# Optimization experiments

Hardware: AMD Instinct MI355X
Metric: run time of the kernel (lower is better)

The kernel has to match this reference:

```python
import jax, jax.numpy as jnp
import numpy as np
import math

DIM, SCALES, ORIENTS, K = 32, 3, 8, 15
SIGMA, GAMMA = 5.0, 0.5
B, H, W = 4, 128, 128

def _make_gabor_filters():
    # matches EnhancedBlockGabor._create_complex_filters
    coords = np.arange(-(K // 2), K // 2 + 1, dtype=np.float32)
    y, x = np.meshgrid(coords, coords, indexing='ij')  # torch.meshgrid default 'ij'
    filts = []
    for s in range(SCALES):
        fu = 1.0 / 2 ** s
        for o in range(ORIENTS):
            theta = o * math.pi / ORIENTS
            xt = x * math.cos(theta) + y * math.sin(theta)
            yt = -x * math.sin(theta) + y * math.cos(theta)
            env = np.exp(-(xt ** 2 + GAMMA ** 2 * yt ** 2) / (2 * SIGMA ** 2))
            amp = fu ** 2 / (math.pi * GAMMA ** 2)
            real = amp * env * np.cos(2 * math.pi * fu * xt)
            imag = amp * env * np.sin(2 * math.pi * fu * xt)
            filts.append(np.stack([real, imag]))
    return jnp.asarray(np.stack(filts), dtype=jnp.float32)  # (S*O, 2, K, K)

def setup_inputs() -> dict:
    key = jax.random.key(0)
    k1, k2, k3 = jax.random.split(key, 3)
    x = jax.random.normal(k1, (B, DIM, H, W), dtype=jnp.float32)
    filters = _make_gabor_filters()
    cin = DIM * SCALES * ORIENTS
    w1 = jax.random.normal(k2, (DIM, cin), dtype=jnp.float32) / np.sqrt(cin)
    b1 = jax.random.normal(k3, (DIM,), dtype=jnp.float32) * 0.01
    return {"x": x, "filters": filters, "w1": w1, "b1": b1}

def reference(x, filters, w1, b1):
    Bb, C, Hh, Ww = x.shape
    SO = filters.shape[0]
    pad = K // 2
    # depthwise multi-scale Gabor conv: every channel vs every (scale,orient,re/im) filter
    xr = x.reshape(Bb * C, 1, Hh, Ww)
    kern = filters.reshape(SO * 2, 1, K, K)
    feat = jax.lax.conv_general_dilated(
        xr, kern, window_strides=(1, 1), padding=[(pad, pad), (pad, pad)],
        dimension_numbers=('NCHW', 'OIHW', 'NCHW'))  # (B*C, SO*2, H, W)
    feat = feat.reshape(Bb, C, SO, 2, Hh, Ww)
    mag = jnp.sqrt(feat[:, :, :, 0] ** 2 + feat[:, :, :, 1] ** 2)  # (B,C,SO,H,W)
    mag = jnp.swapaxes(mag, -1, -2)  # original permutes H<->W before reshape
    mag = mag.reshape(Bb, C * SO, Hh, Ww)
    y = jnp.einsum('oc,bchw->bohw', w1, mag) + b1[None, :, None, None]
    mean = y.mean(axis=(2, 3), keepdims=True)
    var = y.var(axis=(2, 3), keepdims=True)
    return (y - mean) / jnp.sqrt(var + 1e-5)  # InstanceNorm2d (affine=False)
```

## Files before the change

kernel.cpp:

```cpp
#include <hip/hip_runtime.h>


typedef __attribute__((ext_vector_type(8))) short bfx8;
typedef __attribute__((ext_vector_type(4))) float fx4;
typedef __attribute__((ext_vector_type(4))) unsigned ux4;

#define NREP   2
#define RPITCH 144
#define RROWS  144
#define IMG_SH (RROWS * RPITCH)
#define REP_SH (128 * IMG_SH)
#define XREP_SH (NREP * REP_SH)

#define A_OFF    ((size_t)XREP_SH * 2)
#define W1B_OFF  (A_OFF + (size_t)48 * 256 * 2)
#define YP_OFF   (W1B_OFF + (size_t)32 * 32 * 32 * 2)
#define ST_OFF   (YP_OFF + (size_t)128 * 16384 * 4)

#define STG_REP_DW 1296
#define STG_BUF_DW (2 * STG_REP_DW)

__device__ __forceinline__ unsigned short f2bf(float f) {
    unsigned u = __float_as_uint(f);
    u = (u + 0x7FFFu + ((u >> 16) & 1u)) >> 16;
    return (unsigned short)u;
}

__global__ void prep(const float* __restrict__ x, const float* __restrict__ filt,
                     const float* __restrict__ w1, unsigned* __restrict__ xrep,
                     unsigned short* __restrict__ A, unsigned short* __restrict__ w1b,
                     float* __restrict__ stats)
{
    const int bid = blockIdx.x;
    if (bid < 2048) {
        const int DW_PER_ROW = RPITCH / 2;
        const int DW_PER_IMG = IMG_SH / 2;
        const int DW_PER_REP = REP_SH / 2;
        const int total = NREP * DW_PER_REP;
        for (int i = bid * 256 + threadIdx.x; i < total; i += 2048 * 256) {
            int phi  = i / DW_PER_REP;
            int rem  = i - phi * DW_PER_REP;
            int img  = rem / DW_PER_IMG;
            int rem2 = rem - img * DW_PER_IMG;
            int r    = rem2 / DW_PER_ROW;
            int pd   = rem2 - r * DW_PER_ROW;
            int c0   = 2 * pd + phi;
            float v0 = 0.f, v1 = 0.f;
            int rr = r - 7;
            if (rr >= 0 && rr < 128) {
                const float* row = x + ((size_t)img * 128 + rr) * 128;
                int cc0 = c0 - 7;
                if (cc0 >= 0 && cc0 < 128) v0 = row[cc0];
                int cc1 = c0 - 6;
                if (cc1 >= 0 && cc1 < 128) v1 = row[cc1];
            }
            xrep[i] = (unsigned)f2bf(v0) | ((unsigned)f2bf(v1) << 16);
        }
    } else {
        int t = (bid - 2048) * 256 + threadIdx.x;
        if (t < 48 * 256) {
            int f = t >> 8, k = t & 255;
            int ky = k >> 4, kx = k & 15;
            float v = 0.f;
            if (ky < 15 && kx < 15) v = filt[(f * 15 + ky) * 15 + kx];
            A[t] = f2bf(v);
        } else if (t < 48 * 256 + 32 * 32 * 32) {
            int j = t - 48 * 256;
            int c = j >> 10, o = (j >> 5) & 31, so = j & 31;
            float v = (so < 24) ? w1[o * 768 + c * 24 + so] : 0.f;
            w1b[j] = f2bf(v);
        } else if (t < 48 * 256 + 32 * 32 * 32 + 256) {
            stats[t - (48 * 256 + 32 * 32 * 32)] = 0.f;
        }
    }
}

__global__ void __attribute__((amdgpu_waves_per_eu(2, 2)))
__launch_bounds__(256)
conv_mix(const unsigned short* __restrict__ xrep,
         const unsigned short* __restrict__ Aw,
         const unsigned short* __restrict__ w1b,
         float* __restrict__ ypart, float* __restrict__ stats)
{
    __shared__ unsigned stagew[2 * STG_BUF_DW];
    __shared__ unsigned mag_lds[4][32][20];
    __shared__ float stat_lds[4][4][16];

    const int tid  = threadIdx.x;
    const int lane = tid & 63;
    const int wave = tid >> 6;
    const int n    = lane & 15;
    const int q    = lane >> 4;

    const int bid = blockIdx.x;
    const int b   = (bid >> 1) & 3;
    const int h   = (bid & 1) * 64 + (bid >> 3);

    if (lane < 32) {
        ux4 z4 = {0u, 0u, 0u, 0u};
        *(ux4*)&mag_lds[wave][lane][12] = z4;
    }

    ux4 afr[3][8];
#pragma unroll
    for (int mt = 0; mt < 3; ++mt)
#pragma unroll
        for (int s = 0; s < 8; ++s)
            afr[mt][s] = *(const ux4*)(Aw + ((mt * 16 + n) * 256 + s * 32 + q * 8));
#pragma unroll
    for (int mt = 0; mt < 3; ++mt)
#pragma unroll
        for (int s = 0; s < 8; ++s)
            asm volatile("" : "+v"(afr[mt][s]));

    const int px0 = wave * 32;
    const int p   = n & 1;
    const int fbase = p * STG_REP_DW + (q >> 1) * 72 +
                      ((px0 + (n - p) + 8 * (q & 1)) >> 1);

    const int s1p  = (tid + 256) >= 288;
    const int off1 = tid + 256 - (s1p ? 288 : 0);
    const size_t ib0 = ((size_t)(b * 32) * RROWS + h) * RPITCH;

    const fx4 zero4 = {0.f, 0.f, 0.f, 0.f};
    fx4 yacc[2][2];
#pragma unroll
    for (int mt = 0; mt < 2; ++mt)
#pragma unroll
        for (int t = 0; t < 2; ++t) yacc[mt][t] = zero4;

    {
        const unsigned short* g = xrep + ib0;
        ux4 v0 = *(const ux4*)(g + tid * 8);
        ux4 v1 = *(const ux4*)(g + (size_t)s1p * REP_SH + off1 * 8);
        ux4 v2 = {0u, 0u, 0u, 0u};
        if (tid < 64) v2 = *(const ux4*)(g + REP_SH + (tid + 224) * 8);
        *(ux4*)&stagew[tid * 4] = v0;
        *(ux4*)&stagew[s1p * STG_REP_DW + off1 * 4] = v1;
        if (tid < 64) *(ux4*)&stagew[STG_REP_DW + (tid + 224) * 4] = v2;
    }
    __syncthreads();

    for (int c = 0; c < 32; ++c) {
        ux4 nv0, nv1, nv2;
        if (c < 31) {
            const unsigned short* g = xrep + ib0 + (size_t)(c + 1) * IMG_SH;
            nv0 = *(const ux4*)(g + tid * 8);
            nv1 = *(const ux4*)(g + (size_t)s1p * REP_SH + off1 * 8);
            if (tid < 64) nv2 = *(const ux4*)(g + REP_SH + (tid + 224) * 8);
        }

        bfx8 wf[2];
#pragma unroll
        for (int mt = 0; mt < 2; ++mt)
            wf[mt] = *(const bfx8*)(w1b + ((c * 32 + mt * 16 + n) * 32 + q * 8));

        const int fb = (c & 1) * STG_BUF_DW + fbase;
        ux4 braw[2][8];
#pragma unroll
        for (int s = 0; s < 8; ++s)
#pragma unroll
            for (int t = 0; t < 2; ++t) {
                const int ix = fb + s * 144 + t * 8;
                ux4 v = {stagew[ix], stagew[ix + 1], stagew[ix + 2], stagew[ix + 3]};
                braw[t][s] = v;
            }
#pragma unroll
        for (int s = 0; s < 8; ++s)
#pragma unroll
            for (int t = 0; t < 2; ++t)
                asm volatile("" : "+v"(braw[t][s]));

        fx4 cacc[3][2];
#pragma unroll
        for (int mt = 0; mt < 3; ++mt)
#pragma unroll
            for (int t = 0; t < 2; ++t) cacc[mt][t] = zero4;

#pragma unroll
        for (int s = 0; s < 8; ++s)
#pragma unroll
            for (int t = 0; t < 2; ++t) {
                bfx8 bf = __builtin_bit_cast(bfx8, braw[t][s]);
#pragma unroll
                for (int mt = 0; mt < 3; ++mt)
                    cacc[mt][t] = __builtin_amdgcn_mfma_f32_16x16x32_bf16(
                        __builtin_bit_cast(bfx8, afr[mt][s]), bf, cacc[mt][t], 0, 0, 0);
            }

#pragma unroll
        for (int t = 0; t < 2; ++t)
#pragma unroll
            for (int mt = 0; mt < 3; ++mt) {
                float m0 = sqrtf(cacc[mt][t][0] * cacc[mt][t][0] +
                                 cacc[mt][t][1] * cacc[mt][t][1]);
                float m1 = sqrtf(cacc[mt][t][2] * cacc[mt][t][2] +
                                 cacc[mt][t][3] * cacc[mt][t][3]);
                unsigned u0 = __float_as_uint(m0), u1 = __float_as_uint(m1);
                unsigned pk = ((u0 + 0x8000u) >> 16) | ((u1 + 0x8000u) & 0xFFFF0000u);
                mag_lds[wave][t * 16 + n][4 * mt + q] = pk;
            }

#pragma unroll
        for (int t = 0; t < 2; ++t) {
            ux4 raw = *(const ux4*)&mag_lds[wave][t * 16 + n][q * 4];
            bfx8 mb = __builtin_bit_cast(bfx8, raw);
#pragma unroll
            for (int mt = 0; mt < 2; ++mt)
                yacc[mt][t] = __builtin_amdgcn_mfma_f32_16x16x32_bf16(
                    wf[mt], mb, yacc[mt][t], 0, 0, 0);
        }

        if (c < 31) {
            const int wb = ((c + 1) & 1) * STG_BUF_DW;
            *(ux4*)&stagew[wb + tid * 4] = nv0;
            *(ux4*)&stagew[wb + s1p * STG_REP_DW + off1 * 4] = nv1;
            if (tid < 64) *(ux4*)&stagew[wb + STG_REP_DW + (tid + 224) * 4] = nv2;
        }
        __syncthreads();
    }

    float* yp = ypart + (size_t)(b * 32) * 16384 + h * 128;
#pragma unroll
    for (int mt = 0; mt < 2; ++mt)
#pragma unroll
        for (int t = 0; t < 2; ++t) {
            const int w0 = px0 + t * 16 + n;
#pragma unroll
            for (int r = 0; r < 4; ++r)
                yp[(size_t)(mt * 16 + 4 * q + r) * 16384 + w0] = yacc[mt][t][r];
        }

    float sv[8], qv[8];
#pragma unroll
    for (int mt = 0; mt < 2; ++mt)
#pragma unroll
        for (int r = 0; r < 4; ++r) {
            float v0 = yacc[mt][0][r], v1 = yacc[mt][1][r];
            sv[mt * 4 + r] = v0 + v1;
            qv[mt * 4 + r] = v0 * v0 + v1 * v1;
        }
#pragma unroll
    for (int m = 1; m <= 8; m <<= 1)
#pragma unroll
        for (int i = 0; i < 8; ++i) {
            sv[i] += __shfl_xor(sv[i], m);
            qv[i] += __shfl_xor(qv[i], m);
        }
    if (n == 0) {
#pragma unroll
        for (int i = 0; i < 8; ++i) {
            stat_lds[wave][q][i]     = sv[i];
            stat_lds[wave][q][i + 8] = qv[i];
        }
    }
    __syncthreads();
    if (tid < 64) {
        int qq = tid >> 4, i = tid & 15;
        float acc = stat_lds[0][qq][i] + stat_lds[1][qq][i] +
                    stat_lds[2][qq][i] + stat_lds[3][qq][i];
        int kind = i >> 3, mt = (i >> 2) & 1, r = i & 3;
        int o = mt * 16 + 4 * qq + r;
        atomicAdd(&stats[(b * 32 + o) * 2 + kind], acc);
    }
}

__global__ void inorm2(const float* __restrict__ ypart, const float* __restrict__ stats,
                       float* __restrict__ out)
{
    const int bid = blockIdx.x;
    const int bo = bid >> 4, tile = bid & 15;
    const int h0 = (tile >> 2) * 32, w0 = (tile & 3) * 32;
    const float mean = stats[bo * 2] * (1.f / 16384.f);
    float var = stats[bo * 2 + 1] * (1.f / 16384.f) - mean * mean;
    const float rstd = rsqrtf(fmaxf(var, 0.f) + 1e-5f);

    const float* y0 = ypart + (size_t)bo * 16384;
    __shared__ float tilebuf[32][33];
    const int r = threadIdx.x >> 3, c4 = (threadIdx.x & 7) * 4;

    const size_t base = (size_t)(h0 + r) * 128 + w0 + c4;
    fx4 a = *(const fx4*)(y0 + base);
#pragma unroll
    for (int j = 0; j < 4; ++j)
        tilebuf[r][c4 + j] = (a[j] - mean) * rstd;
    __syncthreads();
    float* ob = out + (size_t)bo * 16384 + (size_t)(w0 + r) * 128 + h0 + c4;
    fx4 o4;
#pragma unroll
    for (int j = 0; j < 4; ++j) o4[j] = tilebuf[c4 + j][r];
    *(fx4*)ob = o4;
}

extern "C" void kernel_launch(void* const* d_in, const int* in_sizes, int n_in,
                              void* d_out, int out_size, void* d_ws, size_t ws_size,
                              hipStream_t stream)
{
    const float* x    = (const float*)d_in[0];
    const float* filt = (const float*)d_in[1];
    const float* w1   = (const float*)d_in[2];
    float* out = (float*)d_out;
    char* ws = (char*)d_ws;

    unsigned*       xrep  = (unsigned*)ws;
    unsigned short* Aw    = (unsigned short*)(ws + A_OFF);
    unsigned short* w1b   = (unsigned short*)(ws + W1B_OFF);
    float*          yp    = (float*)(ws + YP_OFF);
    float*          stats = (float*)(ws + ST_OFF);

    prep<<<2048 + 178, 256, 0, stream>>>(x, filt, w1, xrep, Aw, w1b, stats);
    conv_mix<<<512, 256, 0, stream>>>((const unsigned short*)xrep, Aw, w1b, yp, stats);
    inorm2<<<2048, 256, 0, stream>>>(yp, stats, out);
}
```

Measured before the change: 140.1 us.

## Give each wave a private LDS staging window and drop block-wide barriers

Each wave now stages only the input window its 32 pixels need into its own LDS region, with a padded row pitch. This removes the per-channel __syncthreads, since a wave only reads data it wrote itself. Each wave loads a slightly overlapping halo, so global traffic and LDS footprint grow in exchange. The change also swaps sqrtf for a raw v_sqrt_f32, and restructures the prep kernel's indexing to avoid per-element divisions.

```diff
diff --git a/kernel.cpp b/kernel.cpp
--- a/kernel.cpp
+++ b/kernel.cpp
@@ -17,13 +17,21 @@
 #define YP_OFF   (W1B_OFF + (size_t)32 * 32 * 32 * 2)
 #define ST_OFF   (YP_OFF + (size_t)128 * 16384 * 4)
 
-#define STG_REP_DW 1296
-#define STG_BUF_DW (2 * STG_REP_DW)
+#define WROW_DW  40
+#define WREP_DW  656
+#define WBUF_DW  (2 * WREP_DW)
+#define WWAVE_DW (2 * WBUF_DW)
 
 __device__ __forceinline__ unsigned short f2bf(float f) {
     unsigned u = __float_as_uint(f);
     u = (u + 0x7FFFu + ((u >> 16) & 1u)) >> 16;
     return (unsigned short)u;
+}
+
+__device__ __forceinline__ float fsqrt(float x) {
+    float r;
+    asm("v_sqrt_f32 %0, %1" : "=v"(r) : "v"(x));
+    return r;
 }
 
 __global__ void prep(const float* __restrict__ x, const float* __restrict__ filt,
@@ -33,18 +41,14 @@
 {
     const int bid = blockIdx.x;
     if (bid < 2048) {
-        const int DW_PER_ROW = RPITCH / 2;
-        const int DW_PER_IMG = IMG_SH / 2;
-        const int DW_PER_REP = REP_SH / 2;
-        const int total = NREP * DW_PER_REP;
-        for (int i = bid * 256 + threadIdx.x; i < total; i += 2048 * 256) {
-            int phi  = i / DW_PER_REP;
-            int rem  = i - phi * DW_PER_REP;
-            int img  = rem / DW_PER_IMG;
-            int rem2 = rem - img * DW_PER_IMG;
-            int r    = rem2 / DW_PER_ROW;
-            int pd   = rem2 - r * DW_PER_ROW;
-            int c0   = 2 * pd + phi;
+        const int phi = bid & 1, img = (bid >> 1) & 127, rg = bid >> 8;
+        const unsigned obase = (unsigned)phi * (REP_SH / 2) + img * (IMG_SH / 2)
+                             + rg * 18 * 72;
+        for (int j = threadIdx.x; j < 18 * 72; j += 256) {
+            int jr = j / 72;
+            int pd = j - jr * 72;
+            int r  = rg * 18 + jr;
+            int c0 = 2 * pd + phi;
             float v0 = 0.f, v1 = 0.f;
             int rr = r - 7;
             if (rr >= 0 && rr < 128) {
@@ -54,7 +58,7 @@
                 int cc1 = c0 - 6;
                 if (cc1 >= 0 && cc1 < 128) v1 = row[cc1];
             }
-            xrep[i] = (unsigned)f2bf(v0) | ((unsigned)f2bf(v1) << 16);
+            xrep[obase + j] = (unsigned)f2bf(v0) | ((unsigned)f2bf(v1) << 16);
         }
     } else {
         int t = (bid - 2048) * 256 + threadIdx.x;
@@ -82,7 +86,7 @@
          const unsigned short* __restrict__ w1b,
          float* __restrict__ ypart, float* __restrict__ stats)
 {
-    __shared__ unsigned stagew[2 * STG_BUF_DW];
+    __shared__ unsigned stagew[4 * WWAVE_DW];
     __shared__ unsigned mag_lds[4][32][20];
     __shared__ float stat_lds[4][4][16];
 
@@ -115,12 +119,21 @@
 
     const int px0 = wave * 32;
     const int p   = n & 1;
-    const int fbase = p * STG_REP_DW + (q >> 1) * 72 +
-                      ((px0 + (n - p) + 8 * (q & 1)) >> 1);
-
-    const int s1p  = (tid + 256) >= 288;
-    const int off1 = tid + 256 - (s1p ? 288 : 0);
-    const size_t ib0 = ((size_t)(b * 32) * RROWS + h) * RPITCH;
+    const int fbase = wave * WWAVE_DW + p * WREP_DW + (q >> 1) * WROW_DW
+                    + ((n - p) >> 1) + (q & 1) * 4;
+
+    int g_off[3], l_off[3];
+#pragma unroll
+    for (int i = 0; i < 3; ++i) {
+        int slot = i * 64 + lane;
+        int rep  = slot >= 96;
+        int rem  = slot - 96 * rep;
+        int row  = rem / 6;
+        int sl   = rem - row * 6;
+        g_off[i] = rep * REP_SH + (h + row) * RPITCH + px0 + sl * 8;
+        l_off[i] = wave * WWAVE_DW + rep * WREP_DW + row * WROW_DW + sl * 4;
+    }
+    const int imgbase0 = (b * 32) * IMG_SH;
 
     const fx4 zero4 = {0.f, 0.f, 0.f, 0.f};
     fx4 yacc[2][2];
@@ -130,24 +143,19 @@
         for (int t = 0; t < 2; ++t) yacc[mt][t] = zero4;
 
     {
-        const unsigned short* g = xrep + ib0;
-        ux4 v0 = *(const ux4*)(g + tid * 8);
-        ux4 v1 = *(const ux4*)(g + (size_t)s1p * REP_SH + off1 * 8);
-        ux4 v2 = {0u, 0u, 0u, 0u};
-        if (tid < 64) v2 = *(const ux4*)(g + REP_SH + (tid + 224) * 8);
-        *(ux4*)&stagew[tid * 4] = v0;
-        *(ux4*)&stagew[s1p * STG_REP_DW + off1 * 4] = v1;
-        if (tid < 64) *(ux4*)&stagew[STG_REP_DW + (tid + 224) * 4] = v2;
-    }
-    __syncthreads();
+        const unsigned short* g = xrep + imgbase0;
+#pragma unroll
+        for (int i = 0; i < 3; ++i)
+            *(ux4*)&stagew[l_off[i]] = *(const ux4*)(g + g_off[i]);
+    }
 
     for (int c = 0; c < 32; ++c) {
-        ux4 nv0, nv1, nv2;
+        ux4 nv[3];
         if (c < 31) {
-            const unsigned short* g = xrep + ib0 + (size_t)(c + 1) * IMG_SH;
-            nv0 = *(const ux4*)(g + tid * 8);
-            nv1 = *(const ux4*)(g + (size_t)s1p * REP_SH + off1 * 8);
-            if (tid < 64) nv2 = *(const ux4*)(g + REP_SH + (tid + 224) * 8);
+            const unsigned short* g = xrep + imgbase0 + (c + 1) * IMG_SH;
+#pragma unroll
+            for (int i = 0; i < 3; ++i)
+                nv[i] = *(const ux4*)(g + g_off[i]);
         }
 
         bfx8 wf[2];
@@ -155,13 +163,13 @@
         for (int mt = 0; mt < 2; ++mt)
             wf[mt] = *(const bfx8*)(w1b + ((c * 32 + mt * 16 + n) * 32 + q * 8));
 
-        const int fb = (c & 1) * STG_BUF_DW + fbase;
+        const int fb = fbase + (c & 1) * WBUF_DW;
         ux4 braw[2][8];
 #pragma unroll
         for (int s = 0; s < 8; ++s)
 #pragma unroll
             for (int t = 0; t < 2; ++t) {
-                const int ix = fb + s * 144 + t * 8;
+                const int ix = fb + s * (2 * WROW_DW) + t * 8;
                 ux4 v = {stagew[ix], stagew[ix + 1], stagew[ix + 2], stagew[ix + 3]};
                 braw[t][s] = v;
             }
@@ -192,9 +200,9 @@
         for (int t = 0; t < 2; ++t)
 #pragma unroll
             for (int mt = 0; mt < 3; ++mt) {
-                float m0 = sqrtf(cacc[mt][t][0] * cacc[mt][t][0] +
+                float m0 = fsqrt(cacc[mt][t][0] * cacc[mt][t][0] +
                                  cacc[mt][t][1] * cacc[mt][t][1]);
-                float m1 = sqrtf(cacc[mt][t][2] * cacc[mt][t][2] +
+                float m1 = fsqrt(cacc[mt][t][2] * cacc[mt][t][2] +
                                  cacc[mt][t][3] * cacc[mt][t][3]);
                 unsigned u0 = __float_as_uint(m0), u1 = __float_as_uint(m1);
                 unsigned pk = ((u0 + 0x8000u) >> 16) | ((u1 + 0x8000u) & 0xFFFF0000u);
@@ -212,12 +220,11 @@
         }
 
         if (c < 31) {
-            const int wb = ((c + 1) & 1) * STG_BUF_DW;
-            *(ux4*)&stagew[wb + tid * 4] = nv0;
-            *(ux4*)&stagew[wb + s1p * STG_REP_DW + off1 * 4] = nv1;
-            if (tid < 64) *(ux4*)&stagew[wb + STG_REP_DW + (tid + 224) * 4] = nv2;
-        }
-        __syncthreads();
+            const int wb = ((c + 1) & 1) * WBUF_DW;
+#pragma unroll
+            for (int i = 0; i < 3; ++i)
+                *(ux4*)&stagew[wb + l_off[i]] = nv[i];
+        }
     }
 
     float* yp = ypart + (size_t)(b * 32) * 16384 + h * 128;
```

Result: faster. 127.2 us (-9.2%).
